# Optimization experiments

Hardware: AMD Instinct MI355X
Metric: run time of the kernel (lower is better)

Reference implementation:

```python
import jax, jax.numpy as jnp
import numpy as np

B, C, D = 16384, 4096, 512
ALPHA = 0.1
BETA = 0.25


def setup_inputs() -> dict:
    key = jax.random.key(0)
    kx, kc = jax.random.split(key)
    x = jax.random.normal(kx, (B, D), dtype=jnp.float32)
    codes = jax.random.normal(kc, (1, C, D), dtype=jnp.float32)
    return {"x": x, "codes": codes}


def reference(x, codes):
    # x: (B, D), codes: (1, C, D). Eval-mode forward of Quantizer (l2 metric).
    d = x.shape[1]
    c = codes[0]                                  # (C, D)
    # squared l2 distance via expansion (same math as sum((x-c)^2, -1))
    x_sq = jnp.sum(x * x, axis=-1, keepdims=True)  # (B, 1)
    c_sq = jnp.sum(c * c, axis=-1)                 # (C,)
    dots = jnp.einsum('bd,cd->bc', x, c)           # (B, C)
    raw_distances = x_sq + c_sq[None, :] - 2.0 * dots
    distances = raw_distances / d / ALPHA          # scaling preserved for faithfulness
    indices = jnp.argmin(distances, axis=-1)       # (B,)
    quantized = c[indices]                         # (B, D) gather
    # commit loss: dist(x, stop_grad(quantized)); codebook loss: dist(stop_grad(x), quantized)
    diff_commit = x - jax.lax.stop_gradient(quantized)
    loss_commit = jnp.mean(jnp.sum(diff_commit * diff_commit, axis=-1))
    diff_code = jax.lax.stop_gradient(x) - quantized
    loss_codebook = jnp.mean(jnp.sum(diff_code * diff_code, axis=-1))
    loss = loss_commit + BETA * loss_codebook
    return quantized, indices, loss
```

## Files before the change

### kernel.cpp

```cpp
#include <hip/hip_runtime.h>

#define B_SZ 16384
#define C_SZ 4096
#define D_SZ 512

#define QSCALE 22.7f
#define INV_S2 (1.0f / (QSCALE * QSCALE))
#define EPS 6.0f
#define DBIAS 1024.0f

typedef __attribute__((ext_vector_type(4))) int intx4;

__device__ inline unsigned q4(const float4 v) {
    int a = (int)rintf(v.x * QSCALE); a = max(-127, min(127, a));
    int b = (int)rintf(v.y * QSCALE); b = max(-127, min(127, b));
    int c = (int)rintf(v.z * QSCALE); c = max(-127, min(127, c));
    int d = (int)rintf(v.w * QSCALE); d = max(-127, min(127, d));
    return ((unsigned)(a & 255)) | ((unsigned)(b & 255) << 8) |
           ((unsigned)(c & 255) << 16) | ((unsigned)(d & 255) << 24);
}
__device__ inline void gload16(const void* g, void* l) {
    __builtin_amdgcn_global_load_lds(
        (const __attribute__((address_space(1))) void*)g,
        (__attribute__((address_space(3))) void*)l, 16, 0, 0);
}

__global__ __launch_bounds__(256) void convert_kernel(const float* __restrict__ x,
                                                      const float* __restrict__ codes,
                                                      unsigned* __restrict__ xq,
                                                      unsigned* __restrict__ cq,
                                                      float* __restrict__ csq) {
    const int XB = (B_SZ * D_SZ) / 4 / 256;
    if (blockIdx.x < XB) {
        const int tid = blockIdx.x * 256 + threadIdx.x;
        const float4 v = ((const float4*)x)[tid];
        xq[tid] = q4(v);
    } else {
        const int t = threadIdx.x;
        const int wave = t >> 6;
        const int lane = t & 63;
        const int code = (blockIdx.x - XB) * 4 + wave;
        const float4* cp = (const float4*)(codes + (size_t)code * D_SZ);
        float s = 0.0f;
        #pragma unroll
        for (int u = 0; u < 2; ++u) {
            const float4 v = cp[lane + 64 * u];
            cq[(size_t)code * (D_SZ / 4) + lane + 64 * u] = q4(v);
            s = fmaf(v.x, v.x, s); s = fmaf(v.y, v.y, s);
            s = fmaf(v.z, v.z, s); s = fmaf(v.w, v.w, s);
        }
        #pragma unroll
        for (int off = 32; off; off >>= 1) s += __shfl_down(s, off, 64);
        if (lane == 0) csq[code] = s;
    }
}

__global__ __launch_bounds__(512, 4) void gemm_argmin_kernel(
        const unsigned char* __restrict__ xq,
        const unsigned char* __restrict__ cq,
        const float* __restrict__ csq,
        uint2* __restrict__ table) {
    __shared__ unsigned char sA[2][128][64];
    __shared__ unsigned char sB[2][256][64];

    const int t = threadIdx.x;
    const int wave = t >> 6;
    const int lane = t & 63;
    const int quad = lane >> 4;
    const int l15 = lane & 15;
    const int wm = wave >> 2;
    const int wn = wave & 3;

    const int rowbase = blockIdx.y * 128;
    const int colbase = blockIdx.x * 256;

    const int lrow = lane >> 2;
    const int lchunk = (lane & 3) ^ ((lrow >> 1) & 3);
    const unsigned char* gA = xq + (size_t)(rowbase + wave * 16 + lrow) * D_SZ + lchunk * 16;
    const unsigned char* gB = cq + (size_t)(colbase + wave * 32 + lrow) * D_SZ + lchunk * 16;

    const int cc = (quad ^ ((l15 >> 1) & 3)) * 16;

    float cs2[4];
    #pragma unroll
    for (int j = 0; j < 4; ++j)
        cs2[j] = fmaf(0.5f, csq[colbase + wn * 64 + j * 16 + l15], DBIAS);

    intx4 acc[4][4];
    #pragma unroll
    for (int i = 0; i < 4; ++i)
        #pragma unroll
        for (int j = 0; j < 4; ++j) acc[i][j] = (intx4)0;

#define STAGE(d, kt) do { \
        gload16(gA + (kt) * 64,                        &sA[d][wave * 16][0]); \
        gload16(gB + (kt) * 64,                        &sB[d][wave * 32][0]); \
        gload16(gB + (size_t)16 * D_SZ + (kt) * 64,    &sB[d][wave * 32 + 16][0]); \
    } while (0)

#define COMPUTE(d) do { \
        intx4 a[4], b[4]; \
        _Pragma("unroll") for (int i = 0; i < 4; ++i) \
            a[i] = *(const intx4*)&sA[d][wm * 64 + i * 16 + l15][cc]; \
        _Pragma("unroll") for (int j = 0; j < 4; ++j) \
            b[j] = *(const intx4*)&sB[d][wn * 64 + j * 16 + l15][cc]; \
        _Pragma("unroll") for (int i = 0; i < 4; ++i) \
            _Pragma("unroll") for (int j = 0; j < 4; ++j) \
                acc[i][j] = __builtin_amdgcn_mfma_i32_16x16x64_i8(a[i], b[j], acc[i][j], 0, 0, 0); \
    } while (0)

    STAGE(0, 0);
    __syncthreads();

    #pragma unroll
    for (int it = 0; it < 4; ++it) {
        const int kt = it * 2;
        STAGE(1, kt + 1);
        COMPUTE(0);
        __syncthreads();
        if (it < 3) STAGE(0, kt + 2);
        COMPUTE(1);
        __syncthreads();
    }
#undef STAGE
#undef COMPUTE

    const int hb = blockIdx.x * 4 + wn;

    #pragma unroll
    for (int i = 0; i < 4; ++i) {
        #pragma unroll
        for (int r = 0; r < 4; ++r) {
            unsigned k[4];
            #pragma unroll
            for (int j = 0; j < 4; ++j) {
                const float d = fmaf(-(float)acc[i][j][r], INV_S2, cs2[j]);
                k[j] = (__float_as_uint(d) & 0xFFFFFFC0u) | (unsigned)(j * 16 + l15);
            }
            const unsigned lo1 = min(k[0], k[1]), hi1 = max(k[0], k[1]);
            const unsigned lo2 = min(k[2], k[3]), hi2 = max(k[2], k[3]);
            unsigned k1 = min(lo1, lo2);
            unsigned k2 = min(max(lo1, lo2), min(hi1, hi2));
            #pragma unroll
            for (int off = 8; off; off >>= 1) {
                const unsigned ok1 = (unsigned)__shfl_down((int)k1, off, 16);
                const unsigned ok2 = (unsigned)__shfl_down((int)k2, off, 16);
                const unsigned hi = max(k1, ok1);
                const unsigned w2 = (k1 < ok1) ? k2 : ok2;
                k1 = min(k1, ok1);
                k2 = min(hi, w2);
            }
            if (l15 == 0) {
                const int grow = rowbase + wm * 64 + i * 16 + quad * 4 + r;
                table[(size_t)grow * 64 + hb] = make_uint2(k1, k2);
            }
        }
    }
}

__global__ __launch_bounds__(256) void rerank_gather_loss_kernel(
        const float* __restrict__ x,
        const float* __restrict__ codes,
        const float* __restrict__ csq,
        const uint2* __restrict__ table,
        float* __restrict__ outq,
        float* __restrict__ out_idx_f,
        float* __restrict__ partials) {
    __shared__ float red[4];
    const int t = threadIdx.x;
    const int wave = t >> 6;
    const int lane = t & 63;
    const int row0 = (blockIdx.x * 4 + wave) * 4;

    uint2 e[4];
    float4 xv[4][2];
    #pragma unroll
    for (int r = 0; r < 4; ++r) {
        e[r] = table[(size_t)(row0 + r) * 64 + lane];
        const float4* xp = (const float4*)(x + (size_t)(row0 + r) * D_SZ);
        xv[r][0] = xp[lane];
        xv[r][1] = xp[lane + 64];
    }

    int fin[4];
    #pragma unroll
    for (int r = 0; r < 4; ++r) {
        const unsigned k1 = e[r].x, k2 = e[r].y;
        unsigned mk = k1;
        #pragma unroll
        for (int off = 32; off; off >>= 1)
            mk = min(mk, (unsigned)__shfl_xor((int)mk, off, 64));

        const float thr = __uint_as_float(mk & 0xFFFFFFC0u) + EPS;
        const float v1 = __uint_as_float(k1 & 0xFFFFFFC0u);
        const float v2 = __uint_as_float(k2 & 0xFFFFFFC0u);
        const unsigned long long b1 = __ballot(v1 <= thr);
        const unsigned long long b2 = __ballot(v2 <= thr);

        const unsigned long long bm = __ballot(k1 == mk);
        fin[r] = (__ffsll(bm) - 1) * 64 + (int)(mk & 63u);

        if (__popcll(b1) + __popcll(b2) > 1) {
            const int c1 = lane * 64 + (int)(k1 & 63u);
            const int c2 = lane * 64 + (int)(k2 & 63u);
            float bv = 3.4e38f; int bi = 0x7FFFFFFF;
            #pragma unroll
            for (int pass = 0; pass < 2; ++pass) {
                unsigned long long bb = pass ? b2 : b1;
                const int myc = pass ? c2 : c1;
                while (bb) {
                    const int src = __ffsll((unsigned long long)bb) - 1;
                    bb &= bb - 1;
                    const int ci = __shfl(myc, src, 64);
                    const float4* cp = (const float4*)(codes + (size_t)ci * D_SZ);
                    const float4 c0 = cp[lane];
                    const float4 c1v = cp[lane + 64];
                    float s = 0.0f;
                    s = fmaf(xv[r][0].x, c0.x, s);  s = fmaf(xv[r][0].y, c0.y, s);
                    s = fmaf(xv[r][0].z, c0.z, s);  s = fmaf(xv[r][0].w, c0.w, s);
                    s = fmaf(xv[r][1].x, c1v.x, s); s = fmaf(xv[r][1].y, c1v.y, s);
                    s = fmaf(xv[r][1].z, c1v.z, s); s = fmaf(xv[r][1].w, c1v.w, s);
                    #pragma unroll
                    for (int off = 32; off; off >>= 1) s += __shfl_xor(s, off, 64);
                    const float d = fmaf(0.5f, csq[ci], -s);
                    if (d < bv || (d == bv && ci < bi)) { bv = d; bi = ci; }
                }
            }
            fin[r] = bi;
        }
    }

    float4 qv[4][2];
    #pragma unroll
    for (int r = 0; r < 4; ++r) {
        const float4* qp = (const float4*)(codes + (size_t)fin[r] * D_SZ);
        qv[r][0] = qp[lane];
        qv[r][1] = qp[lane + 64];
    }

    float s = 0.0f;
    #pragma unroll
    for (int r = 0; r < 4; ++r) {
        float4* op = (float4*)(outq + (size_t)(row0 + r) * D_SZ);
        op[lane] = qv[r][0];
        op[lane + 64] = qv[r][1];
        const float d0 = xv[r][0].x - qv[r][0].x, d1 = xv[r][0].y - qv[r][0].y;
        const float d2 = xv[r][0].z - qv[r][0].z, d3 = xv[r][0].w - qv[r][0].w;
        const float d4 = xv[r][1].x - qv[r][1].x, d5 = xv[r][1].y - qv[r][1].y;
        const float d6 = xv[r][1].z - qv[r][1].z, d7 = xv[r][1].w - qv[r][1].w;
        s += d0 * d0 + d1 * d1 + d2 * d2 + d3 * d3 + d4 * d4 + d5 * d5 + d6 * d6 + d7 * d7;
        if (lane == 0) out_idx_f[row0 + r] = (float)fin[r];
    }
    #pragma unroll
    for (int off = 32; off; off >>= 1) s += __shfl_down(s, off, 64);
    if (lane == 0) red[wave] = s;
    __syncthreads();
    if (t == 0) partials[blockIdx.x] = red[0] + red[1] + red[2] + red[3];
}

__global__ __launch_bounds__(256) void loss_reduce_kernel(const float* __restrict__ partials,
                                                          float* __restrict__ loss_slot) {
    __shared__ float red[4];
    const int t = threadIdx.x;
    const int wave = t >> 6;
    const int lane = t & 63;
    float s = 0.0f;
    #pragma unroll
    for (int i = 0; i < (B_SZ / 16) / 256; ++i) s += partials[i * 256 + t];
    #pragma unroll
    for (int off = 32; off; off >>= 1) s += __shfl_down(s, off, 64);
    if (lane == 0) red[wave] = s;
    __syncthreads();
    if (t == 0)
        *loss_slot = (red[0] + red[1] + red[2] + red[3]) * (1.25f / (float)B_SZ);
}

extern "C" void kernel_launch(void* const* d_in, const int* in_sizes, int n_in,
                              void* d_out, int out_size, void* d_ws, size_t ws_size,
                              hipStream_t stream) {
    const float* x = (const float*)d_in[0];
    const float* codes = (const float*)d_in[1];

    float* outq = (float*)d_out;
    float* out_idx_f = outq + (size_t)B_SZ * D_SZ;
    float* loss_slot = out_idx_f + B_SZ;

    unsigned char* xq = (unsigned char*)d_ws;
    unsigned char* cq = xq + (size_t)B_SZ * D_SZ;
    float* csq = (float*)(cq + (size_t)C_SZ * D_SZ);
    uint2* table = (uint2*)(csq + C_SZ);
    float* partials = (float*)(table + (size_t)B_SZ * 64);

    const int XB = (B_SZ * D_SZ) / 4 / 256;
    const int CB = C_SZ / 4;
    convert_kernel<<<XB + CB, 256, 0, stream>>>(x, codes, (unsigned*)xq, (unsigned*)cq, csq);
    gemm_argmin_kernel<<<dim3(C_SZ / 256, B_SZ / 128), 512, 0, stream>>>(xq, cq, csq, table);
    rerank_gather_loss_kernel<<<B_SZ / 16, 256, 0, stream>>>(x, codes, csq, table, outq, out_idx_f, partials);
    loss_reduce_kernel<<<1, 256, 0, stream>>>(partials, loss_slot);
}
```

Baseline: 175.1 us.

## Retile int8 distance GEMM to 128x128 blocks with 128-wide K stages

Shrinks the GEMM block tile from 128x256 to 128x128 output and doubles the K depth per LDS stage to 128 bytes, which halves the number of barrier-separated stages. The shared memory becomes one swizzled buffer: four waves load the x tile and four load the code tile. Each wave now owns a 32x64 output sub-tile with half the accumulators, freeing registers and possibly raising occupancy. The cost is lower operand reuse: there are more LDS reads per MFMA and twice as many blocks re-reading x from global memory.

```diff
diff --git a/kernel.cpp b/kernel.cpp
--- a/kernel.cpp
+++ b/kernel.cpp
@@ -60,75 +60,77 @@
         const unsigned char* __restrict__ cq,
         const float* __restrict__ csq,
         uint2* __restrict__ table) {
-    __shared__ unsigned char sA[2][128][64];
-    __shared__ unsigned char sB[2][256][64];
+    __shared__ unsigned char sMem[2][2][128][128];
 
     const int t = threadIdx.x;
     const int wave = t >> 6;
     const int lane = t & 63;
     const int quad = lane >> 4;
     const int l15 = lane & 15;
-    const int wm = wave >> 2;
-    const int wn = wave & 3;
 
     const int rowbase = blockIdx.y * 128;
-    const int colbase = blockIdx.x * 256;
-
-    const int lrow = lane >> 2;
-    const int lchunk = (lane & 3) ^ ((lrow >> 1) & 3);
-    const unsigned char* gA = xq + (size_t)(rowbase + wave * 16 + lrow) * D_SZ + lchunk * 16;
-    const unsigned char* gB = cq + (size_t)(colbase + wave * 32 + lrow) * D_SZ + lchunk * 16;
-
-    const int cc = (quad ^ ((l15 >> 1) & 3)) * 16;
+    const int colbase = blockIdx.x * 128;
+    const int wr = (wave >> 1) * 32;
+    const int wc = (wave & 1) * 64;
+
+    const int ab = (wave < 4) ? 0 : 1;
+    const int rowoff = (wave & 3) * 32;
+    const unsigned char* gsrc = (ab == 0) ? xq + (size_t)rowbase * D_SZ
+                                          : cq + (size_t)colbase * D_SZ;
+    const int lrow = lane >> 3;
+    const int lchunk = (lane & 7) ^ lrow;
+    const unsigned char* gbase = gsrc + (size_t)(rowoff + lrow) * D_SZ + lchunk * 16;
 
     float cs2[4];
     #pragma unroll
     for (int j = 0; j < 4; ++j)
-        cs2[j] = fmaf(0.5f, csq[colbase + wn * 64 + j * 16 + l15], DBIAS);
-
-    intx4 acc[4][4];
-    #pragma unroll
-    for (int i = 0; i < 4; ++i)
+        cs2[j] = fmaf(0.5f, csq[colbase + wc + j * 16 + l15], DBIAS);
+
+    intx4 acc[2][4];
+    #pragma unroll
+    for (int i = 0; i < 2; ++i)
         #pragma unroll
         for (int j = 0; j < 4; ++j) acc[i][j] = (intx4)0;
 
 #define STAGE(d, kt) do { \
-        gload16(gA + (kt) * 64,                        &sA[d][wave * 16][0]); \
-        gload16(gB + (kt) * 64,                        &sB[d][wave * 32][0]); \
-        gload16(gB + (size_t)16 * D_SZ + (kt) * 64,    &sB[d][wave * 32 + 16][0]); \
+        const unsigned char* _g = gbase + (kt) * 128; \
+        _Pragma("unroll") for (int inst = 0; inst < 4; ++inst) \
+            gload16(_g + (size_t)(inst * 8) * D_SZ, &sMem[ab][d][rowoff + inst * 8][0]); \
     } while (0)
 
 #define COMPUTE(d) do { \
-        intx4 a[4], b[4]; \
-        _Pragma("unroll") for (int i = 0; i < 4; ++i) \
-            a[i] = *(const intx4*)&sA[d][wm * 64 + i * 16 + l15][cc]; \
-        _Pragma("unroll") for (int j = 0; j < 4; ++j) \
-            b[j] = *(const intx4*)&sB[d][wn * 64 + j * 16 + l15][cc]; \
-        _Pragma("unroll") for (int i = 0; i < 4; ++i) \
+        _Pragma("unroll") for (int ksub = 0; ksub < 2; ++ksub) { \
+            const int cc = (((ksub * 4 + quad) ^ (l15 & 7))) * 16; \
+            intx4 a[2], b[4]; \
+            _Pragma("unroll") for (int i = 0; i < 2; ++i) \
+                a[i] = *(const intx4*)&sMem[0][d][wr + i * 16 + l15][cc]; \
             _Pragma("unroll") for (int j = 0; j < 4; ++j) \
-                acc[i][j] = __builtin_amdgcn_mfma_i32_16x16x64_i8(a[i], b[j], acc[i][j], 0, 0, 0); \
+                b[j] = *(const intx4*)&sMem[1][d][wc + j * 16 + l15][cc]; \
+            _Pragma("unroll") for (int i = 0; i < 2; ++i) \
+                _Pragma("unroll") for (int j = 0; j < 4; ++j) \
+                    acc[i][j] = __builtin_amdgcn_mfma_i32_16x16x64_i8(a[i], b[j], acc[i][j], 0, 0, 0); \
+        } \
     } while (0)
 
     STAGE(0, 0);
     __syncthreads();
 
     #pragma unroll
-    for (int it = 0; it < 4; ++it) {
-        const int kt = it * 2;
-        STAGE(1, kt + 1);
+    for (int it = 0; it < 2; ++it) {
+        STAGE(1, it * 2 + 1);
         COMPUTE(0);
         __syncthreads();
-        if (it < 3) STAGE(0, kt + 2);
+        if (it < 1) STAGE(0, it * 2 + 2);
         COMPUTE(1);
         __syncthreads();
     }
 #undef STAGE
 #undef COMPUTE
 
-    const int hb = blockIdx.x * 4 + wn;
-
-    #pragma unroll
-    for (int i = 0; i < 4; ++i) {
+    const int hb = blockIdx.x * 2 + (wave & 1);
+
+    #pragma unroll
+    for (int i = 0; i < 2; ++i) {
         #pragma unroll
         for (int r = 0; r < 4; ++r) {
             unsigned k[4];
@@ -151,7 +153,7 @@
                 k2 = min(hi, w2);
             }
             if (l15 == 0) {
-                const int grow = rowbase + wm * 64 + i * 16 + quad * 4 + r;
+                const int grow = rowbase + wr + i * 16 + quad * 4 + r;
                 table[(size_t)grow * 64 + hb] = make_uint2(k1, k2);
             }
         }
@@ -294,7 +296,7 @@
     const int XB = (B_SZ * D_SZ) / 4 / 256;
     const int CB = C_SZ / 4;
     convert_kernel<<<XB + CB, 256, 0, stream>>>(x, codes, (unsigned*)xq, (unsigned*)cq, csq);
-    gemm_argmin_kernel<<<dim3(C_SZ / 256, B_SZ / 128), 512, 0, stream>>>(xq, cq, csq, table);
+    gemm_argmin_kernel<<<dim3(C_SZ / 128, B_SZ / 128), 512, 0, stream>>>(xq, cq, csq, table);
     rerank_gather_loss_kernel<<<B_SZ / 16, 256, 0, stream>>>(x, codes, csq, table, outq, out_idx_f, partials);
     loss_reduce_kernel<<<1, 256, 0, stream>>>(partials, loss_slot);
 }
```

After: 170.7 us. 1.03x faster.
